# Kernel optimization log

Hardware: AMD Instinct MI355X
Metric: run time of the kernel (lower is better)

Reference implementation:

```python
import jax, jax.numpy as jnp
import numpy as np
import math

B, S, D, H, FF, L, V = 4, 2048, 512, 8, 2048, 4, 256
WINDOW, STRIDE, NGLOBAL = 256, 128, 16  # sparse pattern: causal & (local | strided | global)


def setup_inputs() -> dict:
    key = jax.random.key(0)
    ks = jax.random.split(key, 12)
    g = lambda k, shp: jax.random.normal(k, shp, dtype=jnp.float32) * 0.02
    return {
        "src_tokens": jax.random.randint(ks[0], (B, S), 0, V, dtype=jnp.int32),
        "emb": g(ks[1], (V, D)),
        "b_out": jnp.zeros((V,), jnp.float32),
        "Wq": g(ks[2], (L, D, D)), "bq": jnp.zeros((L, D), jnp.float32),
        "Wk": g(ks[3], (L, D, D)), "bk": jnp.zeros((L, D), jnp.float32),
        "Wv": g(ks[4], (L, D, D)), "bv": jnp.zeros((L, D), jnp.float32),
        "Wo": g(ks[5], (L, D, D)), "bo": jnp.zeros((L, D), jnp.float32),
        "ln1_g": jnp.ones((L, D), jnp.float32), "ln1_b": jnp.zeros((L, D), jnp.float32),
        "W1": g(ks[6], (L, D, FF)), "b1": jnp.zeros((L, FF), jnp.float32),
        "W2": g(ks[7], (L, FF, D)), "b2": jnp.zeros((L, D), jnp.float32),
        "ln2_g": jnp.ones((L, D), jnp.float32), "ln2_b": jnp.zeros((L, D), jnp.float32),
    }


def _pos_enc(seq_len, d_model):
    pos = jnp.arange(seq_len, dtype=jnp.float32)[:, None]
    div = jnp.exp(jnp.arange(0, d_model, 2, dtype=jnp.float32) * (-math.log(10000.0) / d_model))
    pe = jnp.zeros((seq_len, d_model), jnp.float32)
    pe = pe.at[:, 0::2].set(jnp.sin(pos * div)).at[:, 1::2].set(jnp.cos(pos * div))
    return pe


def _ln(x, g, b):
    m = x.mean(-1, keepdims=True)
    v = ((x - m) ** 2).mean(-1, keepdims=True)
    return (x - m) * jax.lax.rsqrt(v + 1e-5) * g + b


def _sparse_mask(seq_len):
    i = jnp.arange(seq_len)[:, None]
    j = jnp.arange(seq_len)[None, :]
    causal = j <= i
    local = (i - j) < WINDOW
    strided = ((i - j) % STRIDE) == 0
    glob = j < NGLOBAL
    return causal & (local | strided | glob)  # [S, S] bool


def reference(src_tokens, emb, b_out, Wq, bq, Wk, bk, Wv, bv, Wo, bo,
              ln1_g, ln1_b, W1, b1, W2, b2, ln2_g, ln2_b):
    dh = D // H
    x = emb[src_tokens] * math.sqrt(D) + _pos_enc(S, D)  # [B,S,D] (dropout inactive at eval)
    mask = _sparse_mask(S)
    for l in range(L):
        q = (x @ Wq[l] + bq[l]).reshape(B, S, H, dh)
        k = (x @ Wk[l] + bk[l]).reshape(B, S, H, dh)
        v = (x @ Wv[l] + bv[l]).reshape(B, S, H, dh)
        scores = jnp.einsum('bihd,bjhd->bhij', q, k) / math.sqrt(dh)
        scores = jnp.where(mask, scores, jnp.float32(-1e9))
        attn = jax.nn.softmax(scores, axis=-1)
        o = jnp.einsum('bhij,bjhd->bihd', attn, v).reshape(B, S, D)
        x = _ln(x + o @ Wo[l] + bo[l], ln1_g[l], ln1_b[l])      # post-LN residual
        h = jax.nn.relu(x @ W1[l] + b1[l])
        x = _ln(x + h @ W2[l] + b2[l], ln2_g[l], ln2_b[l])
    return x @ emb.T + b_out  # tied output projection -> [B,S,V]
```

## Files before the change

kernel.cpp:

```cpp
#include <hip/hip_runtime.h>
#include <hip/hip_bf16.h>
#include <math.h>

#define B_  4
#define S_  2048
#define D_  512
#define H_  8
#define DH_ 64
#define FF_ 2048
#define L_  4
#define V_  256
#define NTOK (B_ * S_)
#define XN  ((size_t)NTOK * D_)

typedef __attribute__((ext_vector_type(8))) short bf16x8;
typedef __attribute__((ext_vector_type(4))) float f32x4;
typedef __attribute__((ext_vector_type(8))) unsigned short u16x8;
typedef __attribute__((ext_vector_type(4))) unsigned short u16x4;

typedef const __attribute__((address_space(1))) unsigned int* gptr_u32;
typedef __attribute__((address_space(3))) unsigned int* lptr_u32;

__device__ __forceinline__ float bf2f(unsigned short u) {
    return __uint_as_float((unsigned)u << 16);
}
__device__ __forceinline__ unsigned short f2bf_bits(float f) {
    __hip_bfloat16 t = __float2bfloat16(f);
    return *(unsigned short*)&t;
}

__global__ void pe_table_kernel(float* __restrict__ PE) {
    int s = blockIdx.x;
    int d = threadIdx.x * 2;
    float ang = (float)s * expf((float)d * (-logf(10000.0f) / (float)D_));
    PE[(size_t)s * D_ + d]     = sinf(ang);
    PE[(size_t)s * D_ + d + 1] = cosf(ang);
}

__global__ void embed_kernel(const int* __restrict__ tok,
                             const float* __restrict__ emb,
                             const float* __restrict__ PE,
                             float* __restrict__ X,
                             __hip_bfloat16* __restrict__ Xb) {
    int bs = blockIdx.x;
    int s = bs % S_;
    int t = tok[bs];
    const float scale = 22.62741699796952f;
    int d = threadIdx.x * 4;
    float4 e = *(const float4*)(emb + (size_t)t * D_ + d);
    float4 p = *(const float4*)(PE + (size_t)s * D_ + d);
    float4 v = make_float4(e.x * scale + p.x, e.y * scale + p.y,
                           e.z * scale + p.z, e.w * scale + p.w);
    *(float4*)(X + (size_t)bs * D_ + d) = v;
    u16x4 pk = { f2bf_bits(v.x), f2bf_bits(v.y), f2bf_bits(v.z), f2bf_bits(v.w) };
    *(u16x4*)((unsigned short*)Xb + (size_t)bs * D_ + d) = pk;
}

__global__ void transpose_conv_kernel(const float* __restrict__ W,
                                      __hip_bfloat16* __restrict__ Wt,
                                      int K, int N) {
    const float* Wl = W + (size_t)blockIdx.z * K * N;
    __hip_bfloat16* Wtl = Wt + (size_t)blockIdx.z * K * N;
    __shared__ float t[32][33];
    int k0 = blockIdx.y * 32, n0 = blockIdx.x * 32;
    int tx = threadIdx.x & 31, ty = threadIdx.x >> 5;
    #pragma unroll
    for (int q = 0; q < 4; ++q)
        t[ty + q * 8][tx] = Wl[(size_t)(k0 + ty + q * 8) * N + n0 + tx];
    __syncthreads();
    #pragma unroll
    for (int q = 0; q < 4; ++q)
        Wtl[(size_t)(n0 + ty + q * 8) * K + k0 + tx] =
            __float2bfloat16(t[tx][ty + q * 8]);
}

__global__ void transpose_qkv_kernel(const float* __restrict__ Wq,
                                     const float* __restrict__ Wk,
                                     const float* __restrict__ Wv,
                                     __hip_bfloat16* __restrict__ dst) {
    int z = blockIdx.z, l = z / 3, which = z % 3;
    const float* src = (which == 0 ? Wq : which == 1 ? Wk : Wv) + (size_t)l * D_ * D_;
    __hip_bfloat16* d = dst + (size_t)l * 1536 * D_ + (size_t)which * D_ * D_;
    __shared__ float t[32][33];
    int k0 = blockIdx.y * 32, n0 = blockIdx.x * 32;
    int tx = threadIdx.x & 31, ty = threadIdx.x >> 5;
    #pragma unroll
    for (int q = 0; q < 4; ++q)
        t[ty + q * 8][tx] = src[(size_t)(k0 + ty + q * 8) * D_ + n0 + tx];
    __syncthreads();
    #pragma unroll
    for (int q = 0; q < 4; ++q)
        d[(size_t)(n0 + ty + q * 8) * D_ + k0 + tx] =
            __float2bfloat16(t[tx][ty + q * 8]);
}

__global__ void conv_bf16_kernel(const float* __restrict__ in,
                                 __hip_bfloat16* __restrict__ out, int n) {
    int i = blockIdx.x * 256 + threadIdx.x;
    if (i < n) out[i] = __float2bfloat16(in[i]);
}

template <int BM, int RELU, int OUT_MODE>
__global__ __launch_bounds__(256)
void gemm_bf16_kernel(const __hip_bfloat16* __restrict__ A,
                      const __hip_bfloat16* __restrict__ Bt,
                      const float* __restrict__ bias0,
                      const float* __restrict__ bias1,
                      const float* __restrict__ bias2,
                      float* __restrict__ Cf,
                      __hip_bfloat16* __restrict__ Cb0,
                      __hip_bfloat16* __restrict__ Cb1,
                      __hip_bfloat16* __restrict__ Cb2,
                      __hip_bfloat16* __restrict__ CbT,
                      int M, int N, int K, int lda) {
    constexpr int MI = BM / 32;
    __shared__ unsigned short As[2][BM * 32];
    __shared__ unsigned short Bs[2][128 * 32];
    int tid = threadIdx.x;
    int lane = tid & 63, wid = tid >> 6;
    int wm = (wid >> 1) * (BM / 2), wn = (wid & 1) * 64;
    int g = lane >> 4, il = lane & 15;

    int gx = gridDim.x;
    int fid = blockIdx.x + gx * blockIdx.y;
    int cpx = (gx * gridDim.y) >> 3;
    int swz = (fid & 7) * cpx + (fid >> 3);
    int m0 = (swz / gx) * BM, n0 = (swz % gx) * 128;

    size_t koff = 0;
    if constexpr (OUT_MODE == 5) koff = (size_t)blockIdx.z * K;

    auto stage = [&](int buf, int k0) {
        #pragma unroll
        for (int q = 0; q < BM / 64; ++q) {
            int idx = q * 256 + tid;
            int r = idx >> 2, c = idx & 3;
            int csw = (c ^ r) & 3;
            const __hip_bfloat16* sa = A + (size_t)(m0 + r) * lda + koff + k0 + csw * 8;
            __builtin_amdgcn_global_load_lds((gptr_u32)(const void*)sa,
                                             (lptr_u32)(void*)&As[buf][idx * 8], 16, 0, 0);
        }
        #pragma unroll
        for (int q = 0; q < 2; ++q) {
            int idx = q * 256 + tid;
            int r = idx >> 2, c = idx & 3;
            int csw = (c ^ r) & 3;
            const __hip_bfloat16* sb = Bt + (size_t)(n0 + r) * lda + koff + k0 + csw * 8;
            __builtin_amdgcn_global_load_lds((gptr_u32)(const void*)sb,
                                             (lptr_u32)(void*)&Bs[buf][idx * 8], 16, 0, 0);
        }
    };

    f32x4 acc[MI][4] = {};
    int NT = K >> 5;
    stage(0, 0);

    for (int t = 0; t < NT; ++t) {
        int cur = t & 1;
        if (t + 1 < NT) {
            stage(cur ^ 1, (t + 1) << 5);
            if constexpr (BM == 128)
                asm volatile("s_waitcnt vmcnt(4)" ::: "memory");
            else
                asm volatile("s_waitcnt vmcnt(3)" ::: "memory");
        } else {
            asm volatile("s_waitcnt vmcnt(0)" ::: "memory");
        }
        __builtin_amdgcn_s_barrier();

        bf16x8 af[MI], bf[4];
        #pragma unroll
        for (int i = 0; i < MI; ++i) {
            int m = wm + i * 16 + il;
            af[i] = *(const bf16x8*)&As[cur][m * 32 + ((g ^ m) & 3) * 8];
        }
        #pragma unroll
        for (int j = 0; j < 4; ++j) {
            int n = wn + j * 16 + il;
            bf[j] = *(const bf16x8*)&Bs[cur][n * 32 + ((g ^ n) & 3) * 8];
        }
        #pragma unroll
        for (int i = 0; i < MI; ++i)
            #pragma unroll
            for (int j = 0; j < 4; ++j)
                acc[i][j] = __builtin_amdgcn_mfma_f32_16x16x32_bf16(
                    af[i], bf[j], acc[i][j], 0, 0, 0);

        __builtin_amdgcn_s_barrier();
    }

    if constexpr (OUT_MODE == 4) {
        int seg = n0 >> 9;
        const float* bias = seg == 0 ? bias0 : seg == 1 ? bias1 : bias2;
        __hip_bfloat16* Crow = seg == 0 ? Cb0 : seg == 1 ? Cb1 : Cb2;
        int nseg = n0 & 511;
        #pragma unroll
        for (int j = 0; j < 4; ++j) {
            int coll = nseg + wn + j * 16 + il;
            float bv = bias[coll];
            #pragma unroll
            for (int i = 0; i < MI; ++i) {
                int row0 = m0 + wm + i * 16 + g * 4;
                if (seg < 2) {
                    #pragma unroll
                    for (int r = 0; r < 4; ++r)
                        Crow[(size_t)(row0 + r) * 512 + coll] =
                            __float2bfloat16(acc[i][j][r] + bv);
                } else {
                    u16x4 pk;
                    #pragma unroll
                    for (int r = 0; r < 4; ++r) {
                        float v = acc[i][j][r] + bv;
                        Crow[(size_t)(row0 + r) * 512 + coll] = __float2bfloat16(v);
                        pk[r] = f2bf_bits(v);
                    }
                    int hh = coll >> 6, dh = coll & 63;
                    int bb = row0 >> 11, s0 = row0 & 2047;
                    *(u16x4*)(CbT + ((size_t)((bb * 8 + hh) * 64 + dh) * 2048 + s0)) = pk;
                }
            }
        }
    } else if constexpr (OUT_MODE == 5) {
        __hip_bfloat16* Cd = blockIdx.z ? Cb1 : Cb0;
        #pragma unroll
        for (int j = 0; j < 4; ++j) {
            int col = n0 + wn + j * 16 + il;
            float bv = blockIdx.z ? 0.0f : bias0[col];
            #pragma unroll
            for (int i = 0; i < MI; ++i) {
                #pragma unroll
                for (int r = 0; r < 4; ++r) {
                    int row = m0 + wm + i * 16 + g * 4 + r;
                    Cd[(size_t)row * N + col] = __float2bfloat16(acc[i][j][r] + bv);
                }
            }
        }
    } else {
        #pragma unroll
        for (int j = 0; j < 4; ++j) {
            int col = n0 + wn + j * 16 + il;
            float bv = bias0[col];
            #pragma unroll
            for (int i = 0; i < MI; ++i) {
                #pragma unroll
                for (int r = 0; r < 4; ++r) {
                    int row = m0 + wm + i * 16 + g * 4 + r;
                    float v = acc[i][j][r] + bv;
                    if (RELU) v = fmaxf(v, 0.0f);
                    if (OUT_MODE == 1) Cb0[(size_t)row * N + col] = __float2bfloat16(v);
                    else               Cf[(size_t)row * N + col] = v;
                }
            }
        }
    }
}

__device__ __forceinline__ bf16x8 lds_frag(const unsigned short* base, int row, int chunk) {
    int byte = (row << 7) + (((chunk ^ (row & 7)) & 7) << 4);
    return *(const bf16x8*)((const char*)base + byte);
}

__global__ __launch_bounds__(256)
void attn_mfma_kernel(const __hip_bfloat16* __restrict__ Q,
                      const __hip_bfloat16* __restrict__ K,
                      const __hip_bfloat16* __restrict__ V,
                      const __hip_bfloat16* __restrict__ VT,
                      __hip_bfloat16* __restrict__ O) {
    __shared__ unsigned short SM[4096 + 4096 + 4096];
    unsigned short* Ks = SM;
    unsigned short* Vs = SM + 4096;

    int d = blockIdx.x + 32 * (blockIdx.y + 8 * blockIdx.z);
    int xcd = d & 7;
    int rest = d >> 3;
    int gsub = rest & 3;
    int qt = rest >> 2;
    int grp = xcd * 4 + gsub;
    int h = grp & 7, b = grp >> 3;
    int i0 = qt * 64;

    int tid = threadIdx.x, lane = tid & 63, wv = tid >> 6;
    int g = lane >> 4, il = lane & 15, g4 = g * 4;

    int nloc = min(i0 >> 6, 4) + 1;
    int add0 = (i0 > 256);
    int nt = nloc + add0;

    const size_t vt_off = (size_t)((b * 8 + h) * 64) * 2048;
    auto j0_of = [&](int t) { return (t < nloc) ? (i0 - 64 * t) : 0; };

    auto stage = [&](int j0) {
        #pragma unroll
        for (int q = 0; q < 2; ++q) {
            int idx = q * 256 + tid;
            int row = idx >> 3, c = idx & 7;
            int csw = c ^ (row & 7);
            const __hip_bfloat16* sk = K + (size_t)(b * 2048 + j0 + row) * 512 + h * 64 + csw * 8;
            __builtin_amdgcn_global_load_lds((gptr_u32)(const void*)sk,
                                             (lptr_u32)(void*)&Ks[idx * 8], 16, 0, 0);
            const __hip_bfloat16* sv = VT + vt_off + (size_t)row * 2048 + j0 + csw * 8;
            __builtin_amdgcn_global_load_lds((gptr_u32)(const void*)sv,
                                             (lptr_u32)(void*)&Vs[idx * 8], 16, 0, 0);
        }
    };

    int iq = i0 + wv * 16 + il;
    bf16x8 qf[2];
    #pragma unroll
    for (int kh = 0; kh < 2; ++kh)
        qf[kh] = *(const bf16x8*)(Q + (size_t)(b * 2048 + iq) * 512 + h * 64 + kh * 32 + g * 8);

    stage(j0_of(0));

    float qfl[16];
    #pragma unroll
    for (int kh = 0; kh < 2; ++kh)
        #pragma unroll
        for (int e = 0; e < 8; ++e)
            qfl[kh * 8 + e] = bf2f(((u16x8)qf[kh])[e]);

    unsigned short* myP = SM + 8192 + wv * 1024;
    f32x4 o[4] = {};
    float os[16] = {};
    float m = -1e30f, l = 0.0f;
    const float CSC = 0.18033688011112042f;

    const unsigned short* Kbase = (const unsigned short*)(K + (size_t)b * 2048 * 512 + h * 64);
    const unsigned short* Vbase = (const unsigned short*)(V + (size_t)b * 2048 * 512 + h * 64);
    for (int j = iq - 384; j >= 16; j -= 128) {
        const unsigned short* kr = Kbase + (size_t)j * 512;
        u16x8 k0 = *(const u16x8*)(kr + g * 8);
        u16x8 k1 = *(const u16x8*)(kr + 32 + g * 8);
        float dot = 0.0f;
        #pragma unroll
        for (int e = 0; e < 8; ++e)
            dot += qfl[e] * bf2f(k0[e]) + qfl[8 + e] * bf2f(k1[e]);
        dot += __shfl_xor(dot, 16);
        dot += __shfl_xor(dot, 32);
        float s2 = dot * CSC;
        float mn = fmaxf(m, s2);
        float al = exp2f(m - mn);
        float p = exp2f(s2 - mn);
        l = l * al + p;
        m = mn;
        const unsigned short* vr = Vbase + (size_t)j * 512;
        u16x8 v0 = *(const u16x8*)(vr + g * 8);
        u16x8 v1 = *(const u16x8*)(vr + 32 + g * 8);
        #pragma unroll
        for (int e = 0; e < 8; ++e) {
            os[e]     = os[e]     * al + p * bf2f(v0[e]);
            os[8 + e] = os[8 + e] * al + p * bf2f(v1[e]);
        }
    }

    for (int t = 0; t < nt; ++t) {
        asm volatile("s_waitcnt vmcnt(0)" ::: "memory");
        __builtin_amdgcn_s_barrier();
        int j0 = j0_of(t);
        bool gtile = (t >= nloc);
        bool dtile = (t == 0);

        f32x4 s[4] = {};
        __builtin_amdgcn_s_setprio(1);
        if (gtile) {
            #pragma unroll
            for (int kh = 0; kh < 2; ++kh) {
                bf16x8 a = lds_frag(Ks, il, kh * 4 + g);
                s[0] = __builtin_amdgcn_mfma_f32_16x16x32_bf16(a, qf[kh], s[0], 0, 0, 0);
            }
        } else if (dtile) {
            #pragma unroll
            for (int kh = 0; kh < 2; ++kh)
                #pragma unroll
                for (int jn = 0; jn < 4; ++jn)
                    if (jn <= wv) {
                        bf16x8 a = lds_frag(Ks, jn * 16 + il, kh * 4 + g);
                        s[jn] = __builtin_amdgcn_mfma_f32_16x16x32_bf16(a, qf[kh], s[jn], 0, 0, 0);
                    }
        } else {
            #pragma unroll
            for (int kh = 0; kh < 2; ++kh)
                #pragma unroll
                for (int jn = 0; jn < 4; ++jn) {
                    bf16x8 a = lds_frag(Ks, jn * 16 + il, kh * 4 + g);
                    s[jn] = __builtin_amdgcn_mfma_f32_16x16x32_bf16(a, qf[kh], s[jn], 0, 0, 0);
                }
        }
        __builtin_amdgcn_s_setprio(0);

        float mloc = -1e30f;
        if (gtile) {
            #pragma unroll
            for (int r = 0; r < 4; ++r) {
                float sv = s[0][r] * CSC;
                s[0][r] = sv;
                mloc = fmaxf(mloc, sv);
            }
        } else if (dtile) {
            #pragma unroll
            for (int jn = 0; jn < 4; ++jn) {
                if (jn < wv) {
                    #pragma unroll
                    for (int r = 0; r < 4; ++r) {
                        float sv = s[jn][r] * CSC;
                        s[jn][r] = sv;
                        mloc = fmaxf(mloc, sv);
                    }
                } else if (jn == wv) {
                    #pragma unroll
                    for (int r = 0; r < 4; ++r) {
                        float sv = (g4 + r <= il) ? s[jn][r] * CSC : -1e30f;
                        s[jn][r] = sv;
                        mloc = fmaxf(mloc, sv);
                    }
                }
            }
        } else if (t == 4) {
            #pragma unroll
            for (int jn = 0; jn < 4; ++jn)
                #pragma unroll
                for (int r = 0; r < 4; ++r) {
                    int jg = j0 + jn * 16 + g4 + r;
                    int dij = iq - jg;
                    bool ok = (dij < 256) || ((dij & 127) == 0) || (jg < 16);
                    float sv = ok ? s[jn][r] * CSC : -1e30f;
                    s[jn][r] = sv;
                    mloc = fmaxf(mloc, sv);
                }
        } else {
            #pragma unroll
            for (int jn = 0; jn < 4; ++jn)
                #pragma unroll
                for (int r = 0; r < 4; ++r) {
                    float sv = s[jn][r] * CSC;
                    s[jn][r] = sv;
                    mloc = fmaxf(mloc, sv);
                }
        }
        mloc = fmaxf(mloc, __shfl_xor(mloc, 16));
        mloc = fmaxf(mloc, __shfl_xor(mloc, 32));
        float mn = fmaxf(m, mloc);
        float al = exp2f(m - mn);

        float lloc = 0.0f;
        if (gtile) {
            #pragma unroll
            for (int r = 0; r < 4; ++r) {
                float p = exp2f(s[0][r] - mn);
                s[0][r] = p;
                lloc += p;
            }
        } else {
            #pragma unroll
            for (int jn = 0; jn < 4; ++jn) {
                if (dtile && jn > wv) continue;
                #pragma unroll
                for (int r = 0; r < 4; ++r) {
                    float p = exp2f(s[jn][r] - mn);
                    s[jn][r] = p;
                    lloc += p;
                }
            }
        }
        lloc += __shfl_xor(lloc, 16);
        lloc += __shfl_xor(lloc, 32);
        l = l * al + lloc;
        m = mn;

        if (!__all(al == 1.0f)) {
            float ar[4];
            #pragma unroll
            for (int r = 0; r < 4; ++r) ar[r] = __shfl(al, g4 + r);
            #pragma unroll
            for (int dn = 0; dn < 4; ++dn)
                #pragma unroll
                for (int r = 0; r < 4; ++r) o[dn][r] *= ar[r];
            #pragma unroll
            for (int e = 0; e < 16; ++e) os[e] *= al;
        }

        #pragma unroll
        for (int jn = 0; jn < 4; ++jn) {
            if (gtile && jn >= 2) continue;
            u16x4 pk = { 0, 0, 0, 0 };
            bool live = gtile ? (jn == 0) : (!dtile || jn <= wv);
            if (live) {
                #pragma unroll
                for (int r = 0; r < 4; ++r) pk[r] = f2bf_bits(s[jn][r]);
            }
            int byte = ((il << 7) + (jn << 5) + (g << 3)) ^ ((il & 7) << 4);
            *(u16x4*)((char*)myP + byte) = pk;
        }
        int khmax = (gtile || (dtile && wv < 2)) ? 1 : 2;
        __builtin_amdgcn_s_setprio(1);
        #pragma unroll
        for (int kh = 0; kh < 2; ++kh) {
            if (kh < khmax) {
                bf16x8 pa = lds_frag(myP, il, kh * 4 + g);
                #pragma unroll
                for (int dn = 0; dn < 4; ++dn) {
                    bf16x8 bv = lds_frag(Vs, dn * 16 + il, kh * 4 + g);
                    o[dn] = __builtin_amdgcn_mfma_f32_16x16x32_bf16(pa, bv, o[dn], 0, 0, 0);
                }
            }
        }
        __builtin_amdgcn_s_setprio(0);

        __builtin_amdgcn_s_barrier();
        if (t + 1 < nt) stage(j0_of(t + 1));
    }

    float* osl = (float*)SM + wv * 1024;
    #pragma unroll
    for (int kh = 0; kh < 2; ++kh)
        #pragma unroll
        for (int e = 0; e < 8; ++e)
            osl[il * 64 + kh * 32 + g * 8 + e] = os[kh * 8 + e];
    __syncthreads();

    float li[4];
    #pragma unroll
    for (int r = 0; r < 4; ++r) li[r] = 1.0f / __shfl(l, g4 + r);
    #pragma unroll
    for (int dn = 0; dn < 4; ++dn)
        #pragma unroll
        for (int r = 0; r < 4; ++r) {
            int row = i0 + wv * 16 + g4 + r;
            float add = osl[(g4 + r) * 64 + dn * 16 + il];
            O[(size_t)(b * 2048 + row) * 512 + h * 64 + dn * 16 + il] =
                __float2bfloat16((o[dn][r] + add) * li[r]);
        }
}

__global__ __launch_bounds__(256)
void add_ln_kernel(float* __restrict__ X,
                   const __hip_bfloat16* __restrict__ T1,
                   const __hip_bfloat16* __restrict__ T2,
                   const float* __restrict__ g,
                   const float* __restrict__ bb,
                   __hip_bfloat16* __restrict__ Xb) {
    size_t row = blockIdx.x * 4 + (threadIdx.x >> 6);
    int lane = threadIdx.x & 63;
    int d0 = lane * 8;
    float4 x0 = *(const float4*)(X + row * D_ + d0);
    float4 x1 = *(const float4*)(X + row * D_ + d0 + 4);
    u16x8 t1 = *(const u16x8*)((const unsigned short*)T1 + row * D_ + d0);
    u16x8 t2 = *(const u16x8*)((const unsigned short*)T2 + row * D_ + d0);
    float v[8] = { x0.x + bf2f(t1[0]) + bf2f(t2[0]), x0.y + bf2f(t1[1]) + bf2f(t2[1]),
                   x0.z + bf2f(t1[2]) + bf2f(t2[2]), x0.w + bf2f(t1[3]) + bf2f(t2[3]),
                   x1.x + bf2f(t1[4]) + bf2f(t2[4]), x1.y + bf2f(t1[5]) + bf2f(t2[5]),
                   x1.z + bf2f(t1[6]) + bf2f(t2[6]), x1.w + bf2f(t1[7]) + bf2f(t2[7]) };
    float sum = 0.0f;
    #pragma unroll
    for (int q = 0; q < 8; ++q) sum += v[q];
    #pragma unroll
    for (int o = 32; o; o >>= 1) sum += __shfl_xor(sum, o);
    float mean = sum * (1.0f / D_);
    float var = 0.0f;
    #pragma unroll
    for (int q = 0; q < 8; ++q) { float dd = v[q] - mean; var += dd * dd; }
    #pragma unroll
    for (int o = 32; o; o >>= 1) var += __shfl_xor(var, o);
    var *= (1.0f / D_);
    float r = rsqrtf(var + 1e-5f);
    float4 g0 = *(const float4*)(g + d0),  g1 = *(const float4*)(g + d0 + 4);
    float4 b0 = *(const float4*)(bb + d0), b1 = *(const float4*)(bb + d0 + 4);
    float y[8];
    y[0] = (v[0]-mean)*r*g0.x+b0.x; y[1] = (v[1]-mean)*r*g0.y+b0.y;
    y[2] = (v[2]-mean)*r*g0.z+b0.z; y[3] = (v[3]-mean)*r*g0.w+b0.w;
    y[4] = (v[4]-mean)*r*g1.x+b1.x; y[5] = (v[5]-mean)*r*g1.y+b1.y;
    y[6] = (v[6]-mean)*r*g1.z+b1.z; y[7] = (v[7]-mean)*r*g1.w+b1.w;
    *(float4*)(X + row * D_ + d0)     = make_float4(y[0], y[1], y[2], y[3]);
    *(float4*)(X + row * D_ + d0 + 4) = make_float4(y[4], y[5], y[6], y[7]);
    u16x8 pk;
    #pragma unroll
    for (int q = 0; q < 8; ++q) pk[q] = f2bf_bits(y[q]);
    *(u16x8*)((unsigned short*)Xb + row * D_ + d0) = pk;
}

extern "C" void kernel_launch(void* const* d_in, const int* in_sizes, int n_in,
                              void* d_out, int out_size, void* d_ws, size_t ws_size,
                              hipStream_t stream) {
    const int*   tok   = (const int*)  d_in[0];
    const float* emb   = (const float*)d_in[1];
    const float* b_out = (const float*)d_in[2];
    const float* Wq    = (const float*)d_in[3];
    const float* bq    = (const float*)d_in[4];
    const float* Wk    = (const float*)d_in[5];
    const float* bk    = (const float*)d_in[6];
    const float* Wv    = (const float*)d_in[7];
    const float* bv    = (const float*)d_in[8];
    const float* Wo    = (const float*)d_in[9];
    const float* bo    = (const float*)d_in[10];
    const float* ln1g  = (const float*)d_in[11];
    const float* ln1b  = (const float*)d_in[12];
    const float* W1    = (const float*)d_in[13];
    const float* b1    = (const float*)d_in[14];
    const float* W2    = (const float*)d_in[15];
    const float* b2    = (const float*)d_in[16];
    const float* ln2g  = (const float*)d_in[17];
    const float* ln2b  = (const float*)d_in[18];
    float* out = (float*)d_out;

    char* w = (char*)d_ws;
    auto alloc = [&](size_t bytes) {
        char* p = w;
        w += (bytes + 255) & ~(size_t)255;
        return p;
    };
    float*          X   = (float*)         alloc(XN * 4);
    __hip_bfloat16* Xb  = (__hip_bfloat16*)alloc(XN * 2);
    __hip_bfloat16* Tb  = (__hip_bfloat16*)alloc(XN * 2);
    char* uni = alloc(XN * 2 * 5);
    __hip_bfloat16* Qb  = (__hip_bfloat16*)uni;
    __hip_bfloat16* Kb  = Qb + XN;
    __hip_bfloat16* Vb  = Kb + XN;
    __hip_bfloat16* VTb = Vb + XN;
    __hip_bfloat16* Ob  = VTb + XN;
    __hip_bfloat16* Hb  = (__hip_bfloat16*)uni;
    __hip_bfloat16* T2wo = Qb;
    __hip_bfloat16* T2w2 = Ob;
    __hip_bfloat16* Wqkvt = (__hip_bfloat16*)alloc((size_t)L_ * 1536 * D_ * 2);
    __hip_bfloat16* Wot  = (__hip_bfloat16*)alloc((size_t)L_ * D_ * D_ * 2);
    __hip_bfloat16* W1t  = (__hip_bfloat16*)alloc((size_t)L_ * D_ * FF_ * 2);
    __hip_bfloat16* W2t  = (__hip_bfloat16*)alloc((size_t)L_ * FF_ * D_ * 2);
    __hip_bfloat16* embb = (__hip_bfloat16*)alloc((size_t)V_ * D_ * 2);
    float*          PE   = (float*)alloc((size_t)S_ * D_ * 4);

    {
        pe_table_kernel<<<S_, 256, 0, stream>>>(PE);
        dim3 gqkv(D_ / 32, D_ / 32, L_ * 3);
        transpose_qkv_kernel<<<gqkv, 256, 0, stream>>>(Wq, Wk, Wv, Wqkvt);
        dim3 gdd(D_ / 32, D_ / 32, L_);
        transpose_conv_kernel<<<gdd, 256, 0, stream>>>(Wo, Wot, D_, D_);
        dim3 g1(FF_ / 32, D_ / 32, L_);
        transpose_conv_kernel<<<g1, 256, 0, stream>>>(W1, W1t, D_, FF_);
        dim3 g2(D_ / 32, FF_ / 32, L_);
        transpose_conv_kernel<<<g2, 256, 0, stream>>>(W2, W2t, FF_, D_);
        conv_bf16_kernel<<<(V_ * D_ + 255) / 256, 256, 0, stream>>>(emb, embb, V_ * D_);
    }

    embed_kernel<<<NTOK, 128, 0, stream>>>(tok, emb, PE, X, Xb);

    dim3 blk(256);
    dim3 gqkv(1536 / 128, NTOK / 128);
    dim3 gsplit(D_ / 128, NTOK / 64, 2);
    dim3 gff (FF_ / 128, NTOK / 128);
    dim3 gout(V_ / 128, NTOK / 64);
    dim3 gattn(S_ / 64, H_, B_);
    dim3 gln(NTOK / 4);

    for (int l = 0; l < L_; ++l) {
        const __hip_bfloat16* wqkv = Wqkvt + (size_t)l * 1536 * D_;
        const __hip_bfloat16* wot = Wot + (size_t)l * D_ * D_;
        const __hip_bfloat16* w1t = W1t + (size_t)l * D_ * FF_;
        const __hip_bfloat16* w2t = W2t + (size_t)l * FF_ * D_;

        gemm_bf16_kernel<128, 0, 4><<<gqkv, blk, 0, stream>>>(
            Xb, wqkv, bq + l * D_, bk + l * D_, bv + l * D_,
            nullptr, Qb, Kb, Vb, VTb, NTOK, 1536, D_, D_);

        attn_mfma_kernel<<<gattn, blk, 0, stream>>>(Qb, Kb, Vb, VTb, Ob);

        gemm_bf16_kernel<64, 0, 5><<<gsplit, blk, 0, stream>>>(
            Ob, wot, bo + l * D_, nullptr, nullptr,
            nullptr, Tb, T2wo, nullptr, nullptr, NTOK, D_, 256, D_);
        add_ln_kernel<<<gln, blk, 0, stream>>>(X, Tb, T2wo, ln1g + l * D_, ln1b + l * D_, Xb);

        gemm_bf16_kernel<128, 1, 1><<<gff, blk, 0, stream>>>(
            Xb, w1t, b1 + l * FF_, nullptr, nullptr,
            nullptr, Hb, nullptr, nullptr, nullptr, NTOK, FF_, D_, D_);

        gemm_bf16_kernel<64, 0, 5><<<gsplit, blk, 0, stream>>>(
            Hb, w2t, b2 + l * D_, nullptr, nullptr,
            nullptr, Tb, T2w2, nullptr, nullptr, NTOK, D_, 1024, FF_);
        add_ln_kernel<<<gln, blk, 0, stream>>>(X, Tb, T2w2, ln2g + l * D_, ln2b + l * D_, Xb);
    }

    gemm_bf16_kernel<64, 0, 0><<<gout, blk, 0, stream>>>(
        Xb, embb, b_out, nullptr, nullptr,
        out, nullptr, nullptr, nullptr, nullptr, NTOK, V_, D_, D_);
}
```

Baseline: 656.4 us.

## Split attention KV tiles across two blocks and merge partials in a new kernel

Each query tile's attention work is split into two halves: one block handles the first local tiles, the other handles the remaining tiles plus the scalar strided-key loop. Each half writes unnormalized bf16 partial outputs and its (max, sum) statistics, and a new merge kernel combines them with log-sum-exp rescaling. This doubles the grid to improve occupancy and balance the per-block work. In exchange it adds an extra kernel launch, extra global traffic for the partials, and bf16 rounding of the unnormalized partial outputs.

```diff
diff --git a/kernel.cpp b/kernel.cpp
--- a/kernel.cpp
+++ b/kernel.cpp
@@ -265,7 +265,8 @@
                       const __hip_bfloat16* __restrict__ K,
                       const __hip_bfloat16* __restrict__ V,
                       const __hip_bfloat16* __restrict__ VT,
-                      __hip_bfloat16* __restrict__ O) {
+                      __hip_bfloat16* __restrict__ oP,
+                      float2* __restrict__ mlP) {
     __shared__ unsigned short SM[4096 + 4096 + 4096];
     unsigned short* Ks = SM;
     unsigned short* Vs = SM + 4096;
@@ -274,7 +275,9 @@
     int xcd = d & 7;
     int rest = d >> 3;
     int gsub = rest & 3;
-    int qt = rest >> 2;
+    int r2 = rest >> 2;
+    int half = r2 & 1;
+    int qt = r2 >> 1;
     int grp = xcd * 4 + gsub;
     int h = grp & 7, b = grp >> 3;
     int i0 = qt * 64;
@@ -285,6 +288,11 @@
     int nloc = min(i0 >> 6, 4) + 1;
     int add0 = (i0 > 256);
     int nt = nloc + add0;
+    int nst_max = (i0 + 63 >= 400) ? ((i0 + 63 - 400) >> 7) + 1 : 0;
+    int wTot = nt + (nst_max + 2) / 3;
+    int nsplit = min(nt, (wTot + 1) >> 1);
+    int t0 = half ? nsplit : 0;
+    int t1 = half ? nt : nsplit;
 
     const size_t vt_off = (size_t)((b * 8 + h) * 64) * 2048;
     auto j0_of = [&](int t) { return (t < nloc) ? (i0 - 64 * t) : 0; };
@@ -310,7 +318,7 @@
     for (int kh = 0; kh < 2; ++kh)
         qf[kh] = *(const bf16x8*)(Q + (size_t)(b * 2048 + iq) * 512 + h * 64 + kh * 32 + g * 8);
 
-    stage(j0_of(0));
+    if (t0 < t1) stage(j0_of(t0));
 
     float qfl[16];
     #pragma unroll
@@ -325,35 +333,37 @@
     float m = -1e30f, l = 0.0f;
     const float CSC = 0.18033688011112042f;
 
-    const unsigned short* Kbase = (const unsigned short*)(K + (size_t)b * 2048 * 512 + h * 64);
-    const unsigned short* Vbase = (const unsigned short*)(V + (size_t)b * 2048 * 512 + h * 64);
-    for (int j = iq - 384; j >= 16; j -= 128) {
-        const unsigned short* kr = Kbase + (size_t)j * 512;
-        u16x8 k0 = *(const u16x8*)(kr + g * 8);
-        u16x8 k1 = *(const u16x8*)(kr + 32 + g * 8);
-        float dot = 0.0f;
-        #pragma unroll
-        for (int e = 0; e < 8; ++e)
-            dot += qfl[e] * bf2f(k0[e]) + qfl[8 + e] * bf2f(k1[e]);
-        dot += __shfl_xor(dot, 16);
-        dot += __shfl_xor(dot, 32);
-        float s2 = dot * CSC;
-        float mn = fmaxf(m, s2);
-        float al = exp2f(m - mn);
-        float p = exp2f(s2 - mn);
-        l = l * al + p;
-        m = mn;
-        const unsigned short* vr = Vbase + (size_t)j * 512;
-        u16x8 v0 = *(const u16x8*)(vr + g * 8);
-        u16x8 v1 = *(const u16x8*)(vr + 32 + g * 8);
-        #pragma unroll
-        for (int e = 0; e < 8; ++e) {
-            os[e]     = os[e]     * al + p * bf2f(v0[e]);
-            os[8 + e] = os[8 + e] * al + p * bf2f(v1[e]);
+    if (half) {
+        const unsigned short* Kbase = (const unsigned short*)(K + (size_t)b * 2048 * 512 + h * 64);
+        const unsigned short* Vbase = (const unsigned short*)(V + (size_t)b * 2048 * 512 + h * 64);
+        for (int j = iq - 384; j >= 16; j -= 128) {
+            const unsigned short* kr = Kbase + (size_t)j * 512;
+            u16x8 k0 = *(const u16x8*)(kr + g * 8);
+            u16x8 k1 = *(const u16x8*)(kr + 32 + g * 8);
+            float dot = 0.0f;
+            #pragma unroll
+            for (int e = 0; e < 8; ++e)
+                dot += qfl[e] * bf2f(k0[e]) + qfl[8 + e] * bf2f(k1[e]);
+            dot += __shfl_xor(dot, 16);
+            dot += __shfl_xor(dot, 32);
+            float s2 = dot * CSC;
+            float mn = fmaxf(m, s2);
+            float al = exp2f(m - mn);
+            float p = exp2f(s2 - mn);
+            l = l * al + p;
+            m = mn;
+            const unsigned short* vr = Vbase + (size_t)j * 512;
+            u16x8 v0 = *(const u16x8*)(vr + g * 8);
+            u16x8 v1 = *(const u16x8*)(vr + 32 + g * 8);
+            #pragma unroll
+            for (int e = 0; e < 8; ++e) {
+                os[e]     = os[e]     * al + p * bf2f(v0[e]);
+                os[8 + e] = os[8 + e] * al + p * bf2f(v1[e]);
+            }
         }
     }
 
-    for (int t = 0; t < nt; ++t) {
+    for (int t = t0; t < t1; ++t) {
         asm volatile("s_waitcnt vmcnt(0)" ::: "memory");
         __builtin_amdgcn_s_barrier();
         int j0 = j0_of(t);
@@ -507,9 +517,10 @@
         __builtin_amdgcn_s_setprio(0);
 
         __builtin_amdgcn_s_barrier();
-        if (t + 1 < nt) stage(j0_of(t + 1));
+        if (t + 1 < t1) stage(j0_of(t + 1));
     }
 
+    __syncthreads();
     float* osl = (float*)SM + wv * 1024;
     #pragma unroll
     for (int kh = 0; kh < 2; ++kh)
@@ -518,18 +529,35 @@
             osl[il * 64 + kh * 32 + g * 8 + e] = os[kh * 8 + e];
     __syncthreads();
 
-    float li[4];
-    #pragma unroll
-    for (int r = 0; r < 4; ++r) li[r] = 1.0f / __shfl(l, g4 + r);
+    size_t pbase = ((size_t)(half * 32 + grp) * 2048);
     #pragma unroll
     for (int dn = 0; dn < 4; ++dn)
         #pragma unroll
         for (int r = 0; r < 4; ++r) {
             int row = i0 + wv * 16 + g4 + r;
             float add = osl[(g4 + r) * 64 + dn * 16 + il];
-            O[(size_t)(b * 2048 + row) * 512 + h * 64 + dn * 16 + il] =
-                __float2bfloat16((o[dn][r] + add) * li[r]);
-        }
+            oP[(pbase + row) * 64 + dn * 16 + il] = __float2bfloat16(o[dn][r] + add);
+        }
+    if (g == 0) mlP[pbase + iq] = make_float2(m, l);
+}
+
+__global__ __launch_bounds__(256)
+void attn_merge_kernel(const __hip_bfloat16* __restrict__ oP,
+                       const float2* __restrict__ mlP,
+                       __hip_bfloat16* __restrict__ O) {
+    int row = blockIdx.x * 4 + (threadIdx.x >> 6);
+    int lane = threadIdx.x & 63;
+    float2 A = mlP[row];
+    float2 Bm = mlP[65536 + row];
+    float ms = fmaxf(A.x, Bm.x);
+    float aA = exp2f(A.x - ms), aB = exp2f(Bm.x - ms);
+    float ls = A.y * aA + Bm.y * aB;
+    float oA = bf2f(((const unsigned short*)oP)[(size_t)row * 64 + lane]);
+    float oB = bf2f(((const unsigned short*)oP)[((size_t)65536 + row) * 64 + lane]);
+    float ov = (oA * aA + oB * aB) / ls;
+    int bh = row >> 11, s = row & 2047;
+    int b = bh >> 3, h = bh & 7;
+    O[((size_t)(b * 2048 + s)) * 512 + h * 64 + lane] = __float2bfloat16(ov);
 }
 
 __global__ __launch_bounds__(256)
@@ -626,6 +654,8 @@
     __hip_bfloat16* W2t  = (__hip_bfloat16*)alloc((size_t)L_ * FF_ * D_ * 2);
     __hip_bfloat16* embb = (__hip_bfloat16*)alloc((size_t)V_ * D_ * 2);
     float*          PE   = (float*)alloc((size_t)S_ * D_ * 4);
+    __hip_bfloat16* oP   = (__hip_bfloat16*)alloc((size_t)2 * 32 * 2048 * 64 * 2);
+    float2*         mlP  = (float2*)alloc((size_t)2 * 32 * 2048 * 8);
 
     {
         pe_table_kernel<<<S_, 256, 0, stream>>>(PE);
@@ -647,7 +677,7 @@
     dim3 gsplit(D_ / 128, NTOK / 64, 2);
     dim3 gff (FF_ / 128, NTOK / 128);
     dim3 gout(V_ / 128, NTOK / 64);
-    dim3 gattn(S_ / 64, H_, B_);
+    dim3 gattn(S_ / 64, H_, 2 * B_);
     dim3 gln(NTOK / 4);
 
     for (int l = 0; l < L_; ++l) {
@@ -660,7 +690,8 @@
             Xb, wqkv, bq + l * D_, bk + l * D_, bv + l * D_,
             nullptr, Qb, Kb, Vb, VTb, NTOK, 1536, D_, D_);
 
-        attn_mfma_kernel<<<gattn, blk, 0, stream>>>(Qb, Kb, Vb, VTb, Ob);
+        attn_mfma_kernel<<<gattn, blk, 0, stream>>>(Qb, Kb, Vb, VTb, oP, mlP);
+        attn_merge_kernel<<<65536 / 4, blk, 0, stream>>>(oP, mlP, Ob);
 
         gemm_bf16_kernel<64, 0, 5><<<gsplit, blk, 0, stream>>>(
             Ob, wot, bo + l * D_, nullptr, nullptr,
```

After: 693.1 us. +5.6%, slower.
